# Optimization experiments

Hardware: AMD Instinct MI355X
Metric: run time of the kernel (lower is better)

## Reference

```python
import jax, jax.numpy as jnp
import numpy as np

N_HEADS = 64
N_KV_HEADS = 8
HEAD_DIM = 128
HIDDEN = 8192
SEQ = 2048


def setup_inputs() -> dict:
    key = jax.random.key(0)
    k1, k2, k3, k4 = jax.random.split(key, 4)
    scale = 1.0 / np.sqrt(HIDDEN)
    x = jax.random.normal(k1, (1, 1, SEQ, HIDDEN), dtype=jnp.float32)
    wq = jax.random.normal(k2, (HIDDEN, N_HEADS * HEAD_DIM), dtype=jnp.float32) * scale
    wk = jax.random.normal(k3, (HIDDEN, N_KV_HEADS * HEAD_DIM), dtype=jnp.float32) * scale
    wv = jax.random.normal(k4, (HIDDEN, N_KV_HEADS * HEAD_DIM), dtype=jnp.float32) * scale
    return {"x": x, "wq": wq, "wk": wk, "wv": wv}


def reference(x, wq, wk, wv):
    # Fused QKV projection: concat weights along output dim, single matmul.
    qkv_w = jnp.concatenate([wq, wk, wv], axis=-1)  # [H, (64+8+8)*128]
    fused = jnp.einsum('bush,hd->busd', x, qkv_w)    # [1,1,S,10240]
    b, _, s, _ = fused.shape
    q_dim = N_HEADS * HEAD_DIM
    kv_dim = N_KV_HEADS * HEAD_DIM
    q = fused[..., :q_dim]
    k = fused[..., q_dim:q_dim + kv_dim]
    v = fused[..., q_dim + kv_dim:]
    # nlp_create_qkv_heads: [B,1,S,nh*hd] -> [B,nh,S,hd]
    q_heads = q.reshape(b, s, N_HEADS, HEAD_DIM).transpose(0, 2, 1, 3)
    k_heads = k.reshape(b, s, N_KV_HEADS, HEAD_DIM).transpose(0, 2, 1, 3)
    v_heads = v.reshape(b, s, N_KV_HEADS, HEAD_DIM).transpose(0, 2, 1, 3)
    return (q_heads, k_heads, v_heads)
```

## Files before the change

kernel.cpp:

```cpp
#include <hip/hip_runtime.h>
#include <stdint.h>

#define M_DIM 2048
#define K_DIM 8192
#define N_Q   8192
#define N_KV  1024
#define N_TOT (N_Q + 2 * N_KV)
#define BM    128
#define BN    128
#define BK    32
#define NIT   (K_DIM / BK)

typedef __bf16 bf16x8 __attribute__((ext_vector_type(8)));
typedef __bf16 bf16x2 __attribute__((ext_vector_type(2)));
typedef float  f32x4  __attribute__((ext_vector_type(4)));

__global__ __launch_bounds__(256) void xcast(const float* __restrict__ x,
                                             __bf16* __restrict__ xb) {
    size_t i = ((size_t)blockIdx.x * 256 + threadIdx.x) * 8;
    f32x4 a = *(const f32x4*)(x + i);
    f32x4 b = *(const f32x4*)(x + i + 4);
    bf16x8 o = { (__bf16)a.x, (__bf16)a.y, (__bf16)a.z, (__bf16)a.w,
                 (__bf16)b.x, (__bf16)b.y, (__bf16)b.z, (__bf16)b.w };
    *(bf16x8*)(xb + i) = o;
}

__global__ __launch_bounds__(256) void wcast_t(const float* __restrict__ wq,
                                               const float* __restrict__ wk,
                                               const float* __restrict__ wv,
                                               __bf16* __restrict__ wt) {
    __shared__ float sT[64 * 65];
    const uint32_t bid   = blockIdx.x;
    const uint32_t ktile = bid & 127;
    const uint32_t ntile = bid >> 7;
    const float* W; uint32_t ldW, csrc, cdst;
    if (ntile < 128)      { W = wq; ldW = N_Q;  csrc = ntile * 64;
                            cdst = csrc; }
    else if (ntile < 144) { W = wk; ldW = N_KV; csrc = (ntile - 128) * 64;
                            cdst = N_Q + csrc; }
    else                  { W = wv; ldW = N_KV; csrc = (ntile - 144) * 64;
                            cdst = N_Q + N_KV + csrc; }
    const uint32_t k0 = ktile * 64;
    const uint32_t t  = threadIdx.x;

    const uint32_t lr = t >> 4;
    const uint32_t lc = (t & 15) * 4;
    const float* gp = W + (size_t)(k0 + lr) * ldW + csrc + lc;
    #pragma unroll
    for (int i = 0; i < 4; ++i) {
        f32x4 v = *(const f32x4*)(gp + (size_t)i * 16 * ldW);
        float* d = &sT[(lr + i * 16) * 65 + lc];
        d[0] = v.x; d[1] = v.y; d[2] = v.z; d[3] = v.w;
    }
    __syncthreads();

    const uint32_t wn  = t >> 3;
    const uint32_t wk8 = (t & 7) * 8;
    #pragma unroll
    for (int it = 0; it < 2; ++it) {
        uint32_t n = wn + it * 32;
        bf16x8 o;
        #pragma unroll
        for (int j = 0; j < 8; ++j) o[j] = (__bf16)sT[(wk8 + j) * 65 + n];
        *(bf16x8*)(wt + (size_t)(cdst + n) * K_DIM + k0 + wk8) = o;
    }
}

__device__ __forceinline__ void gload16(const void* g, void* l) {
    __builtin_amdgcn_global_load_lds(
        (const __attribute__((address_space(1))) void*)g,
        (__attribute__((address_space(3))) void*)l, 16, 0, 0);
}

__global__ __launch_bounds__(256) void qkv_mm(const __bf16* __restrict__ xb,
                                              const __bf16* __restrict__ wt,
                                              float* __restrict__ out) {
    __shared__ __align__(16) __bf16 sA[2][BM * BK];
    __shared__ __align__(16) __bf16 sB[2][BN * BK];

    const uint32_t tid = threadIdx.x;

    const uint32_t logical = (blockIdx.x & 7) * 160 + (blockIdx.x >> 3);
    const uint32_t mt = logical & 15;
    const uint32_t nt = logical >> 4;
    const uint32_t m0 = mt * BM;
    const uint32_t n0 = nt * BN;

    const uint32_t w    = tid >> 6;
    const uint32_t lane = tid & 63;
    const __bf16* gA[2];
    const __bf16* gB[2];
    #pragma unroll
    for (int i = 0; i < 2; ++i) {
        uint32_t c  = w * 128 + i * 64 + lane;
        uint32_t r  = c >> 2;
        uint32_t qs = (c & 3) ^ ((r >> 1) & 3);
        gA[i] = xb + (size_t)(m0 + r) * K_DIM + qs * 8;
        gB[i] = wt + (size_t)(n0 + r) * K_DIM + qs * 8;
    }
    char* laA[2]; char* laB[2];
    #pragma unroll
    for (int b = 0; b < 2; ++b) {
        laA[b] = (char*)(&sA[b][0]) + w * 2048;
        laB[b] = (char*)(&sB[b][0]) + w * 2048;
    }

    const uint32_t wm   = (w >> 1) * 64;
    const uint32_t wn   = (w & 1) * 64;
    const uint32_t l15  = lane & 15;
    const uint32_t quad = lane >> 4;

    uint32_t a_off[4], b_off[4];
    #pragma unroll
    for (int t = 0; t < 4; ++t) {
        uint32_t ar = wm + t * 16 + l15;
        a_off[t] = ar * BK + ((quad ^ ((ar >> 1) & 3)) * 8);
        uint32_t br = wn + t * 16 + l15;
        b_off[t] = br * BK + ((quad ^ ((br >> 1) & 3)) * 8);
    }

    f32x4 acc[4][4] = {};

    gload16(gA[0], laA[0]); gload16(gA[1], laA[0] + 1024);
    gload16(gB[0], laB[0]); gload16(gB[1], laB[0] + 1024);
    gA[0] += BK; gA[1] += BK; gB[0] += BK; gB[1] += BK;
    __syncthreads();

    uint32_t cur = 0;
    for (uint32_t kt = 0; kt < NIT; ++kt) {
        const uint32_t nxt = cur ^ 1;
        if (kt + 1 < NIT) {
            gload16(gA[0], laA[nxt]); gload16(gA[1], laA[nxt] + 1024);
            gload16(gB[0], laB[nxt]); gload16(gB[1], laB[nxt] + 1024);
            gA[0] += BK; gA[1] += BK; gB[0] += BK; gB[1] += BK;
        }

        const __bf16* pA = &sA[cur][0];
        const __bf16* pB = &sB[cur][0];
        bf16x8 af[4], bfr[4];
        #pragma unroll
        for (int t = 0; t < 4; ++t) {
            af[t]  = *(const bf16x8*)(pA + a_off[t]);
            bfr[t] = *(const bf16x8*)(pB + b_off[t]);
        }
        #pragma unroll
        for (int mi = 0; mi < 4; ++mi)
            #pragma unroll
            for (int ni = 0; ni < 4; ++ni)
                acc[mi][ni] = __builtin_amdgcn_mfma_f32_16x16x32_bf16(
                    af[mi], bfr[ni], acc[mi][ni], 0, 0, 0);

        __syncthreads();
        cur = nxt;
    }

    float* op = out + (size_t)nt * (M_DIM * 128) + (size_t)m0 * 128;
    #pragma unroll
    for (int mi = 0; mi < 4; ++mi) {
        #pragma unroll
        for (int r = 0; r < 4; ++r) {
            uint32_t row = wm + mi * 16 + quad * 4 + r;
            #pragma unroll
            for (int ni = 0; ni < 4; ++ni) {
                uint32_t col = wn + ni * 16 + l15;
                op[(size_t)row * 128 + col] = acc[mi][ni][r];
            }
        }
    }
}

__device__ __forceinline__ uint32_t swz_fb(uint32_t r) { return ((r >> 1) ^ (r >> 3)) & 3u; }

__device__ __forceinline__ uint32_t pack_bf16(float lo, float hi) {
    bf16x2 v = { (__bf16)lo, (__bf16)hi };
    return __builtin_bit_cast(uint32_t, v);
}

__global__ __launch_bounds__(256) void qkv_gemm(
    const float* __restrict__ x,
    const float* __restrict__ wq,
    const float* __restrict__ wk,
    const float* __restrict__ wv,
    float* __restrict__ out)
{
    __shared__ __align__(16) uint16_t sA[BM * BK];
    __shared__ __align__(16) uint16_t sB[BN * BK];
    uint32_t* sAu = (uint32_t*)sA;
    uint32_t* sBu = (uint32_t*)sB;

    const uint32_t tid    = threadIdx.x;
    const uint32_t bid    = blockIdx.x;
    const uint32_t mt_blk = bid & 15;
    const uint32_t nt_blk = bid >> 4;
    const uint32_t m0     = mt_blk * BM;

    const size_t QSZ = (size_t)64 * M_DIM * 128;
    const size_t KSZ = (size_t)8  * M_DIM * 128;
    const float* Wsel;
    uint32_t ldW, col0;
    size_t obase;
    if (nt_blk < 64)      { Wsel = wq; ldW = N_Q;  col0 = nt_blk * 128;
                            obase = (size_t)nt_blk * M_DIM * 128; }
    else if (nt_blk < 72) { Wsel = wk; ldW = N_KV; col0 = (nt_blk - 64) * 128;
                            obase = QSZ + (size_t)(nt_blk - 64) * M_DIM * 128; }
    else                  { Wsel = wv; ldW = N_KV; col0 = (nt_blk - 72) * 128;
                            obase = QSZ + KSZ + (size_t)(nt_blk - 72) * M_DIM * 128; }

    const float* agp = x + (size_t)(m0 + (tid >> 3)) * K_DIM + (tid & 7) * 4;
    uint32_t a_wr[4];
    #pragma unroll
    for (int i = 0; i < 4; ++i) {
        uint32_t r = i * 32 + (tid >> 3);
        a_wr[i] = r * 16 + ((((tid >> 1) & 3) ^ swz_fb(r)) * 4) + (tid & 1) * 2;
    }

    const uint32_t bk  = (tid >> 4) * 2;
    const uint32_t bn0 = (tid & 15) * 8;
    const float* bgp = Wsel + (size_t)bk * ldW + col0 + bn0;
    const uint32_t bkc = bk >> 3;
    const uint32_t bkd = (bk & 7) >> 1;

    f32x4 apre[4], bpre[4];
    #pragma unroll
    for (int i = 0; i < 4; ++i) apre[i] = *(const f32x4*)(agp + (size_t)i * 32 * K_DIM);
    bpre[0] = *(const f32x4*)(bgp);
    bpre[1] = *(const f32x4*)(bgp + 4);
    bpre[2] = *(const f32x4*)(bgp + ldW);
    bpre[3] = *(const f32x4*)(bgp + ldW + 4);

    const uint32_t lane = tid & 63;
    const uint32_t wid  = tid >> 6;
    const uint32_t wm   = (wid >> 1) * 64;
    const uint32_t wn   = (wid & 1) * 64;
    const uint32_t l15  = lane & 15;
    const uint32_t quad = lane >> 4;

    f32x4 acc[4][4] = {};

    uint32_t a_off[4], b_off[4];
    #pragma unroll
    for (int t = 0; t < 4; ++t) {
        uint32_t ar = wm + t * 16 + l15;
        a_off[t] = ar * BK + ((quad ^ swz_fb(ar)) * 8);
        uint32_t br = wn + t * 16 + l15;
        b_off[t] = br * BK + ((quad ^ swz_fb(br)) * 8);
    }

    const float* agp_n = agp + BK;
    const float* bgp_n = bgp + (size_t)BK * ldW;

    for (uint32_t kt = 0; kt < NIT; ++kt) {
        __syncthreads();

        #pragma unroll
        for (int i = 0; i < 4; ++i) {
            uint2 wv2;
            wv2.x = pack_bf16(apre[i].x, apre[i].y);
            wv2.y = pack_bf16(apre[i].z, apre[i].w);
            *(uint2*)&sAu[a_wr[i]] = wv2;
        }
        {
            const float* pk0 = (const float*)&bpre[0];
            const float* pk1 = (const float*)&bpre[2];
            #pragma unroll
            for (int j = 0; j < 8; ++j) {
                uint32_t n = bn0 + j;
                sBu[n * 16 + ((bkc ^ swz_fb(n)) * 4) + bkd] = pack_bf16(pk0[j], pk1[j]);
            }
        }

        if (kt + 1 < NIT) {
            #pragma unroll
            for (int i = 0; i < 4; ++i) apre[i] = *(const f32x4*)(agp_n + (size_t)i * 32 * K_DIM);
            bpre[0] = *(const f32x4*)(bgp_n);
            bpre[1] = *(const f32x4*)(bgp_n + 4);
            bpre[2] = *(const f32x4*)(bgp_n + ldW);
            bpre[3] = *(const f32x4*)(bgp_n + ldW + 4);
            agp_n += BK;
            bgp_n += (size_t)BK * ldW;
        }

        __syncthreads();

        bf16x8 af[4], bf[4];
        #pragma unroll
        for (int t = 0; t < 4; ++t) {
            af[t] = *(const bf16x8*)(sA + a_off[t]);
            bf[t] = *(const bf16x8*)(sB + b_off[t]);
        }
        #pragma unroll
        for (int mi = 0; mi < 4; ++mi)
            #pragma unroll
            for (int ni = 0; ni < 4; ++ni)
                acc[mi][ni] = __builtin_amdgcn_mfma_f32_16x16x32_bf16(
                    af[mi], bf[ni], acc[mi][ni], 0, 0, 0);
    }

    float* op = out + obase + (size_t)m0 * 128;
    #pragma unroll
    for (int mi = 0; mi < 4; ++mi) {
        #pragma unroll
        for (int r = 0; r < 4; ++r) {
            uint32_t row = wm + mi * 16 + quad * 4 + r;
            #pragma unroll
            for (int ni = 0; ni < 4; ++ni) {
                uint32_t col = wn + ni * 16 + l15;
                op[(size_t)row * 128 + col] = acc[mi][ni][r];
            }
        }
    }
}

extern "C" void kernel_launch(void* const* d_in, const int* in_sizes, int n_in,
                              void* d_out, int out_size, void* d_ws, size_t ws_size,
                              hipStream_t stream) {
    const float* x  = (const float*)d_in[0];
    const float* wq = (const float*)d_in[1];
    const float* wk = (const float*)d_in[2];
    const float* wv = (const float*)d_in[3];

    const size_t XB_BYTES = (size_t)M_DIM * K_DIM * 2;
    const size_t WT_BYTES = (size_t)N_TOT * K_DIM * 2;

    if (ws_size >= XB_BYTES + WT_BYTES) {
        __bf16* xb = (__bf16*)d_ws;
        __bf16* wt = (__bf16*)((char*)d_ws + XB_BYTES);
        xcast<<<dim3((M_DIM * K_DIM) / (256 * 8)), dim3(256), 0, stream>>>(x, xb);
        wcast_t<<<dim3((K_DIM / 64) * (N_TOT / 64)), dim3(256), 0, stream>>>(wq, wk, wv, wt);
        qkv_mm<<<dim3((M_DIM / BM) * (N_TOT / BN)), dim3(256), 0, stream>>>(xb, wt, (float*)d_out);
    } else {
        qkv_gemm<<<dim3((M_DIM / BM) * (N_TOT / BN)), dim3(256), 0, stream>>>(
            x, wq, wk, wv, (float*)d_out);
    }
}
```

Measured before the change: 916.1 us.

## Switch GEMM main loop to three-stage LDS pipeline with vmcnt waits

Replaces the double-buffered LDS scheme with a triple buffer, so two tiles are prefetched ahead and global-to-LDS loads get more time to complete. Each iteration does a single barrier after waiting with s_waitcnt vmcnt for the oldest stage only, in place of a full syncthreads after the MFMA block. This cuts barrier count and exposes more memory latency hiding. In exchange LDS use rises by half, which can lower occupancy, and correctness now depends on the hand-written vmcnt counts matching the four loads per stage.

```diff
diff --git a/kernel.cpp b/kernel.cpp
--- a/kernel.cpp
+++ b/kernel.cpp
@@ -72,11 +72,13 @@
         (__attribute__((address_space(3))) void*)l, 16, 0, 0);
 }
 
+#define TILE_ELTS (BM * BK)
+
 __global__ __launch_bounds__(256) void qkv_mm(const __bf16* __restrict__ xb,
                                               const __bf16* __restrict__ wt,
                                               float* __restrict__ out) {
-    __shared__ __align__(16) __bf16 sA[2][BM * BK];
-    __shared__ __align__(16) __bf16 sB[2][BN * BK];
+    __shared__ __align__(16) __bf16 sA[3][TILE_ELTS];
+    __shared__ __align__(16) __bf16 sB[3][TILE_ELTS];
 
     const uint32_t tid = threadIdx.x;
 
@@ -98,9 +100,9 @@
         gA[i] = xb + (size_t)(m0 + r) * K_DIM + qs * 8;
         gB[i] = wt + (size_t)(n0 + r) * K_DIM + qs * 8;
     }
-    char* laA[2]; char* laB[2];
-    #pragma unroll
-    for (int b = 0; b < 2; ++b) {
+    char* laA[3]; char* laB[3];
+    #pragma unroll
+    for (int b = 0; b < 3; ++b) {
         laA[b] = (char*)(&sA[b][0]) + w * 2048;
         laB[b] = (char*)(&sB[b][0]) + w * 2048;
     }
@@ -121,22 +123,30 @@
 
     f32x4 acc[4][4] = {};
 
-    gload16(gA[0], laA[0]); gload16(gA[1], laA[0] + 1024);
-    gload16(gB[0], laB[0]); gload16(gB[1], laB[0] + 1024);
-    gA[0] += BK; gA[1] += BK; gB[0] += BK; gB[1] += BK;
-    __syncthreads();
-
-    uint32_t cur = 0;
+    auto STAGE = [&](uint32_t b) {
+        gload16(gA[0], laA[b]); gload16(gA[1], laA[b] + 1024);
+        gload16(gB[0], laB[b]); gload16(gB[1], laB[b] + 1024);
+        gA[0] += BK; gA[1] += BK; gB[0] += BK; gB[1] += BK;
+    };
+
+    STAGE(0);
+    STAGE(1);
+
+    uint32_t rd = 0;
     for (uint32_t kt = 0; kt < NIT; ++kt) {
-        const uint32_t nxt = cur ^ 1;
         if (kt + 1 < NIT) {
-            gload16(gA[0], laA[nxt]); gload16(gA[1], laA[nxt] + 1024);
-            gload16(gB[0], laB[nxt]); gload16(gB[1], laB[nxt] + 1024);
-            gA[0] += BK; gA[1] += BK; gB[0] += BK; gB[1] += BK;
-        }
-
-        const __bf16* pA = &sA[cur][0];
-        const __bf16* pB = &sB[cur][0];
+            asm volatile("s_waitcnt vmcnt(4)" ::: "memory");
+        } else {
+            asm volatile("s_waitcnt vmcnt(0)" ::: "memory");
+        }
+        __builtin_amdgcn_sched_barrier(0);
+        __builtin_amdgcn_s_barrier();
+        __builtin_amdgcn_sched_barrier(0);
+
+        if (kt + 2 < NIT) STAGE(rd >= 1 ? rd - 1 : 2);
+
+        const __bf16* pA = &sA[rd][0];
+        const __bf16* pB = &sB[rd][0];
         bf16x8 af[4], bfr[4];
         #pragma unroll
         for (int t = 0; t < 4; ++t) {
@@ -150,8 +160,7 @@
                 acc[mi][ni] = __builtin_amdgcn_mfma_f32_16x16x32_bf16(
                     af[mi], bfr[ni], acc[mi][ni], 0, 0, 0);
 
-        __syncthreads();
-        cur = nxt;
+        rd = (rd == 2) ? 0 : rd + 1;
     }
 
     float* op = out + (size_t)nt * (M_DIM * 128) + (size_t)m0 * 128;
```

New measurement: 955.7 us. 1.04x slower.
